# Kernel optimization log

Hardware: AMD Instinct MI355X
Metric: run time of the kernel (lower is better)

Reference implementation:

```python
import jax, jax.numpy as jnp
import numpy as np

K = 16       # hidden size k
STATE = 8    # state_size

def _pre(x, W1, b1, W2, b2):
    # PreProcess: two Linear+ReLU layers
    return jax.nn.relu(jax.nn.relu(x @ W1 + b1) @ W2 + b2)

def _dblock(x, W1, b1, W2, b2, Wmu, bmu, Wls, bls):
    # DBlock (TD-VAE style): gated hidden then mu / logsigma heads
    t = jnp.tanh(x @ W1 + b1) * jax.nn.sigmoid(x @ W2 + b2)
    return t @ Wmu + bmu, t @ Wls + bls

def setup_inputs() -> dict:
    key = jax.random.key(0)
    ks = iter(jax.random.split(key, 40))
    L, B, IN, OBS = 1000, 1024, 8, 4
    def w(shape):
        return (jax.random.normal(next(ks), shape, jnp.float32) / np.sqrt(shape[0])).astype(jnp.float32)
    z = lambda n: jnp.zeros((n,), jnp.float32)
    return {
        "external_input_seq": jax.random.normal(next(ks), (L, B, IN), jnp.float32),
        "observations_seq":   jax.random.normal(next(ks), (L, B, OBS), jnp.float32),
        "eps":                jax.random.normal(next(ks), (L, B, STATE), jnp.float32),
        # process_u / process_x / process_z (PreProcess)
        "pu_W1": w((IN, K)),  "pu_b1": z(K), "pu_W2": w((K, K)), "pu_b2": z(K),
        "px_W1": w((OBS, K)), "px_b1": z(K), "px_W2": w((K, K)), "px_b2": z(K),
        "pz_W1": w((STATE, K)), "pz_b1": z(K), "pz_W2": w((K, K)), "pz_b2": z(K),
        # posterior_gauss: DBlock(3k, 3k, state_size)
        "post_W1": w((3*K, 3*K)), "post_b1": z(3*K),
        "post_W2": w((3*K, 3*K)), "post_b2": z(3*K),
        "post_Wmu": w((3*K, STATE)), "post_bmu": z(STATE),
        "post_Wls": w((3*K, STATE)), "post_bls": z(STATE),
        # rnn: tanh RNN cell, input 3k -> hidden k, 1 layer
        "rnn_Wih": w((3*K, K)), "rnn_bih": z(K),
        "rnn_Whh": w((K, K)),   "rnn_bhh": z(K),
    }

def reference(external_input_seq, observations_seq, eps,
              pu_W1, pu_b1, pu_W2, pu_b2,
              px_W1, px_b1, px_W2, px_b2,
              pz_W1, pz_b1, pz_W2, pz_b2,
              post_W1, post_b1, post_W2, post_b2,
              post_Wmu, post_bmu, post_Wls, post_bls,
              rnn_Wih, rnn_bih, rnn_Whh, rnn_bhh):
    # forward_posterior with memory_state=None
    L, B, _ = external_input_seq.shape
    u_e = _pre(external_input_seq, pu_W1, pu_b1, pu_W2, pu_b2)  # [L,B,K] (precomputed, as in torch)
    x_e = _pre(observations_seq, px_W1, px_b1, px_W2, px_b2)    # [L,B,K]
    h0 = jnp.zeros((B, K), external_input_seq.dtype)

    def step(h, inputs):
        xe_t, ue_t, eps_t = inputs  # [B,K],[B,K],[B,STATE]
        mu, ls = _dblock(jnp.concatenate([xe_t, ue_t, h], -1),
                         post_W1, post_b1, post_W2, post_b2,
                         post_Wmu, post_bmu, post_Wls, post_bls)
        # reparameterized sample from N(mu, diag(exp(ls))) -> std = exp(0.5*ls)
        z_t = mu + jnp.exp(0.5 * ls) * eps_t
        z_e = _pre(z_t, pz_W1, pz_b1, pz_W2, pz_b2)
        rnn_in = jnp.concatenate([xe_t, ue_t, z_e], -1)  # [B,3K]
        h_new = jnp.tanh(rnn_in @ rnn_Wih + rnn_bih + h @ rnn_Whh + rnn_bhh)
        return h_new, (mu, ls)

    h_final, (state_mu, state_logsigma) = jax.lax.scan(step, h0, (x_e, u_e, eps))
    # returns (state_mu, state_logsigma, memory_state hn); rnn_hidden == hn[None] for 1 layer
    return state_mu, state_logsigma, h_final
```

## Files before the change

kernel.cpp:

```cpp
#include <hip/hip_runtime.h>

#define L_STEPS 1000
#define BATCH   1024
#define REC     128

__device__ __forceinline__ float frcp(float x)  { return __builtin_amdgcn_rcpf(x); }
__device__ __forceinline__ float fsig(float x)  { return frcp(1.0f + __expf(-x)); }
__device__ __forceinline__ float ftanh(float x) { return 1.0f - 2.0f * frcp(__expf(2.0f * x) + 1.0f); }

__device__ __forceinline__ float qxor1(float x) {
    return __int_as_float(__builtin_amdgcn_update_dpp(0, __float_as_int(x), 0xB1, 0xF, 0xF, true));
}
__device__ __forceinline__ float qxor2(float x) {
    return __int_as_float(__builtin_amdgcn_update_dpp(0, __float_as_int(x), 0x4E, 0xF, 0xF, true));
}

#define FMA4(vv, W, base, A) do { \
    A = fmaf((vv).x, W[(base)+0], A); \
    A = fmaf((vv).y, W[(base)+1], A); \
    A = fmaf((vv).z, W[(base)+2], A); \
    A = fmaf((vv).w, W[(base)+3], A); } while (0)

__global__ __launch_bounds__(128) void vrnn_pre(
    const float* __restrict__ ext, const float* __restrict__ obs,
    const float* __restrict__ puW1, const float* __restrict__ pub1,
    const float* __restrict__ puW2, const float* __restrict__ pub2,
    const float* __restrict__ pxW1, const float* __restrict__ pxb1,
    const float* __restrict__ pxW2, const float* __restrict__ pxb2,
    const float* __restrict__ poW1, const float* __restrict__ pob1,
    const float* __restrict__ poW2, const float* __restrict__ pob2,
    const float* __restrict__ Wih, const float* __restrict__ bih,
    const float* __restrict__ bhh,
    float* __restrict__ ws)
{
    const int j  = threadIdx.x;
    const int rc = blockIdx.x * 128;
    const int t  = blockIdx.y;

    __shared__ float wsm[768];
    __shared__ float xu[128][36];

    for (int i = j; i < 64;  i += 128) wsm[0   + i] = pxW1[i];
    for (int i = j; i < 256; i += 128) wsm[64  + i] = pxW2[i];
    for (int i = j; i < 128; i += 128) wsm[320 + i] = puW1[i];
    for (int i = j; i < 256; i += 128) wsm[448 + i] = puW2[i];
    if (j < 16) {
        wsm[704 + j] = pxb1[j]; wsm[720 + j] = pxb2[j];
        wsm[736 + j] = pub1[j]; wsm[752 + j] = pub2[j];
    }
    __syncthreads();

    {
        const size_t row = (size_t)t * BATCH + rc + j;
        const float* o = obs + row * 4;
        const float* e = ext + row * 8;
        float ob[4], ex[8];
        #pragma unroll
        for (int k = 0; k < 4; ++k) ob[k] = o[k];
        #pragma unroll
        for (int k = 0; k < 8; ++k) ex[k] = e[k];

        float t1[16];
        #pragma unroll
        for (int c = 0; c < 16; ++c) {
            float a = wsm[704 + c];
            #pragma unroll
            for (int k = 0; k < 4; ++k) a = fmaf(ob[k], wsm[0 + k * 16 + c], a);
            t1[c] = fmaxf(a, 0.0f);
        }
        #pragma unroll
        for (int c = 0; c < 16; ++c) {
            float a = wsm[720 + c];
            #pragma unroll
            for (int k = 0; k < 16; ++k) a = fmaf(t1[k], wsm[64 + k * 16 + c], a);
            xu[j][c] = fmaxf(a, 0.0f);
        }
        #pragma unroll
        for (int c = 0; c < 16; ++c) {
            float a = wsm[736 + c];
            #pragma unroll
            for (int k = 0; k < 8; ++k) a = fmaf(ex[k], wsm[320 + k * 16 + c], a);
            t1[c] = fmaxf(a, 0.0f);
        }
        #pragma unroll
        for (int c = 0; c < 16; ++c) {
            float a = wsm[752 + c];
            #pragma unroll
            for (int k = 0; k < 16; ++k) a = fmaf(t1[k], wsm[448 + k * 16 + c], a);
            xu[j][16 + c] = fmaxf(a, 0.0f);
        }
    }

    float wc[32]; float bias = 0.0f;
    if (j < 96) {
        const int c = j >> 1;
        const float* W = (j & 1) ? poW2 : poW1;
        bias = (j & 1) ? pob2[c] : pob1[c];
        #pragma unroll
        for (int k = 0; k < 32; ++k) wc[k] = W[k * 48 + c];
    } else if (j < 112) {
        const int c = j - 96;
        bias = bih[c] + bhh[c];
        #pragma unroll
        for (int k = 0; k < 32; ++k) wc[k] = Wih[k * 16 + c];
    } else {
        #pragma unroll
        for (int k = 0; k < 32; ++k) wc[k] = 0.0f;
    }
    __syncthreads();

    float* rb = ws + ((size_t)t * BATCH + rc) * REC + j;
    for (int r = 0; r < 128; ++r) {
        const float4* x4 = (const float4*)&xu[r][0];
        float a = bias;
        #pragma unroll
        for (int q = 0; q < 8; ++q) { float4 v = x4[q]; FMA4(v, wc, 4 * q, a); }
        rb[(size_t)r * REC] = a;
    }
}

__global__ __launch_bounds__(64, 1) void vrnn_scan2(
    const float* __restrict__ ws, const float* __restrict__ eps,
    const float* __restrict__ poW1, const float* __restrict__ poW2,
    const float* __restrict__ Wmu, const float* __restrict__ bmu,
    const float* __restrict__ Wls, const float* __restrict__ bls,
    const float* __restrict__ pzW1, const float* __restrict__ pzb1,
    const float* __restrict__ pzW2, const float* __restrict__ pzb2,
    const float* __restrict__ Wih, const float* __restrict__ Whh,
    float* __restrict__ out)
{
    const int l   = threadIdx.x;
    const int r   = blockIdx.x;
    const int idx = l >> 2;
    const int p   = l & 3;

    const int cl = (l < 48) ? l : 47;
    float wAh[16], wBh[16];
    #pragma unroll
    for (int k = 0; k < 16; ++k) {
        wAh[k] = poW1[(32 + k) * 48 + cl];
        wBh[k] = poW2[(32 + k) * 48 + cl];
    }
    const int hm = idx & 7;
    const float* WH = (idx < 8) ? Wmu : Wls;
    float whead[12];
    #pragma unroll
    for (int i = 0; i < 12; ++i) whead[i] = WH[(12 * p + i) * 8 + hm];
    const float bhead = (idx < 8) ? bmu[hm] : bls[hm];

    float wr[8];
    #pragma unroll
    for (int i = 0; i < 8; ++i)
        wr[i] = (p < 2) ? Wih[(32 + 8 * (p & 1) + i) * 16 + idx]
                        : Whh[(8 * (p & 1) + i) * 16 + idx];

    const float wz1a = pzW1[(2 * p) * 16 + idx];
    const float wz1b = pzW1[(2 * p + 1) * 16 + idx];
    const float bz1  = pzb1[idx];
    float wz2[4];
    #pragma unroll
    for (int i = 0; i < 4; ++i) wz2[i] = pzW2[(4 * p + i) * 16 + idx];
    const float bz2 = pzb2[idx];

    const float* recp = ws + (size_t)r * REC + ((l < 48) ? 2 * l : 48 + l);
    const size_t rstride = (size_t)BATCH * REC;
    const float* epsp = eps + (size_t)r * 8 + (l & 7);

    float2 f2 = make_float2(0.0f, 0.0f); float d1 = 0.0f;
    if (l < 48) f2 = *(const float2*)recp; else d1 = *recp;
    float ev = *epsp;
    recp += rstride; epsp += (size_t)8 * BATCH;

    float* pout = out + ((idx < 8) ? ((size_t)r * 8 + idx)
                                   : ((size_t)L_STEPS * BATCH * 8 + (size_t)r * 8 + (idx - 8)));

    float h[16];
    #pragma unroll
    for (int k = 0; k < 16; ++k) h[k] = 0.0f;
    float hn = 0.0f;

    for (int t = 0; t < L_STEPS; ++t) {
        const float s1p = f2.x, s2p = f2.y;
        const float ihpv = d1, epsv = ev;

        float2 nf2 = make_float2(0.0f, 0.0f); float nd1 = 0.0f;
        if (l < 48) nf2 = *(const float2*)recp; else nd1 = *recp;
        float nev = *epsp;
        recp += (t < L_STEPS - 2) ? rstride : 0;
        epsp += (t < L_STEPS - 2) ? (size_t)8 * BATCH : 0;

        const float ihg = __shfl(ihpv, 48 + idx);
        const float eg  = __shfl(epsv, idx & 7);

        #pragma unroll
        for (int k = 0; k < 16; ++k) h[k] = __shfl(hn, 4 * k);
        float sA = s1p, sB = s2p;
        #pragma unroll
        for (int k = 0; k < 16; ++k) {
            sA = fmaf(h[k], wAh[k], sA);
            sB = fmaf(h[k], wBh[k], sB);
        }
        const float tt = ftanh(sA) * fsig(sB);

        float acc = 0.0f;
        #pragma unroll
        for (int i = 0; i < 12; ++i) acc = fmaf(__shfl(tt, 12 * p + i), whead[i], acc);
        acc += qxor1(acc); acc += qxor2(acc);
        acc += bhead;
        if (p == 0) *pout = acc;
        pout += (size_t)8 * BATCH;

        const float other = __shfl(acc, l ^ 32);
        const float zv = fmaf(__expf(0.5f * other), eg, acc);

        float a1 = fmaf(__shfl(zv, 8 * p), wz1a, __shfl(zv, 8 * p + 4) * wz1b);
        a1 += qxor1(a1); a1 += qxor2(a1);
        a1 = fmaxf(a1 + bz1, 0.0f);

        float ze = 0.0f;
        #pragma unroll
        for (int i = 0; i < 4; ++i) ze = fmaf(__shfl(a1, 16 * p + 4 * i), wz2[i], ze);
        ze += qxor1(ze); ze += qxor2(ze);
        ze = fmaxf(ze + bz2, 0.0f);

        float pre = 0.0f;
        #pragma unroll
        for (int i = 0; i < 8; ++i) {
            const float g = __shfl(ze, 4 * (8 * (p & 1) + i));
            const float v = (p < 2) ? g : h[8 * (p & 1) + i];
            pre = fmaf(v, wr[i], pre);
        }
        pre += qxor1(pre); pre += qxor2(pre);
        hn = ftanh(pre + ihg);

        f2 = nf2; d1 = nd1; ev = nev;
    }

    if (p == 0) out[(size_t)L_STEPS * BATCH * 8 * 2 + (size_t)r * 16 + idx] = hn;
}

__global__ __launch_bounds__(64, 1) void vrnn_scan(
    const float* __restrict__ ext, const float* __restrict__ obs, const float* __restrict__ eps,
    const float* __restrict__ puW1, const float* __restrict__ pub1,
    const float* __restrict__ puW2, const float* __restrict__ pub2,
    const float* __restrict__ pxW1, const float* __restrict__ pxb1,
    const float* __restrict__ pxW2, const float* __restrict__ pxb2,
    const float* __restrict__ pzW1, const float* __restrict__ pzb1,
    const float* __restrict__ pzW2, const float* __restrict__ pzb2,
    const float* __restrict__ poW1, const float* __restrict__ pob1,
    const float* __restrict__ poW2, const float* __restrict__ pob2,
    const float* __restrict__ Wmu, const float* __restrict__ bmu,
    const float* __restrict__ Wls, const float* __restrict__ bls,
    const float* __restrict__ Wih, const float* __restrict__ bih,
    const float* __restrict__ Whh, const float* __restrict__ bhh,
    float* __restrict__ out)
{
    const int l   = threadIdx.x;
    const int r   = blockIdx.x;
    const int idx = l >> 2;
    const int p   = l & 3;

    __shared__ __align__(16) float rawbuf[16];
    __shared__ __align__(16) float epsbuf[8];
    __shared__ __align__(16) float h1buf[32];
    __shared__ __align__(16) float in64[64];
    __shared__ __align__(16) float s2buf[48];
    __shared__ __align__(16) float t48[48];
    __shared__ __align__(16) float zbuf[8];
    __shared__ __align__(16) float ze1buf[16];
    __shared__ float bheadb[16];
    __shared__ float brnnb[16];

    if (l < 16) {
        rawbuf[l]    = 0.0f;
        in64[48 + l] = 0.0f;
        bheadb[l]    = (l < 8) ? bmu[l] : bls[l - 8];
        brnnb[l]     = bih[l] + bhh[l];
    }

    float wA[48]; float biasA;
    {
        const float* baseA;
        if (l < 48) { baseA = poW1 + l;        biasA = pob1[l]; }
        else        { baseA = poW2 + (l - 48); biasA = pob2[l - 48]; }
        #pragma unroll
        for (int k = 0; k < 48; ++k) wA[k] = baseA[k * 48];
    }
    float wB[48]; float biasB;
    {
        const int c = 16 + (l & 31);
        const float* baseB = poW2 + c;
        biasB = pob2[c];
        #pragma unroll
        for (int k = 0; k < 48; ++k) wB[k] = baseB[k * 48];
    }
    float whead[12];
    {
        const float* baseH = (idx < 8) ? (Wmu + idx) : (Wls + (idx - 8));
        #pragma unroll
        for (int i = 0; i < 12; ++i) whead[i] = baseH[(12 * p + i) * 8];
    }
    float wrnn[16];
    {
        #pragma unroll
        for (int i = 0; i < 16; ++i) {
            const int c = 16 * p + i;
            const float a = Wih[min(c, 47) * 16 + idx];
            const float b = Whh[max(c - 48, 0) * 16 + idx];
            wrnn[i] = (c < 48) ? a : b;
        }
    }
    const int j16 = l & 15;
    float wpre1[8], wpre2[16], bpre1, bpre2;
    {
        const bool isx = (l < 16);
        #pragma unroll
        for (int k = 0; k < 8; ++k) {
            const float xv = pxW1[min(k, 3) * 16 + j16];
            const float uv = puW1[k * 16 + j16];
            float v = isx ? xv : uv;
            if (isx && k >= 4) v = 0.0f;
            wpre1[k] = v;
        }
        #pragma unroll
        for (int k = 0; k < 16; ++k) {
            const float xv = pxW2[k * 16 + j16];
            const float uv = puW2[k * 16 + j16];
            wpre2[k] = isx ? xv : uv;
        }
        bpre1 = isx ? pxb1[j16] : pub1[j16];
        bpre2 = isx ? pxb2[j16] : pub2[j16];
    }
    float wpz1[8], wpz2[16], bpz1, bpz2;
    {
        #pragma unroll
        for (int k = 0; k < 8; ++k)  wpz1[k] = pzW1[k * 16 + j16];
        #pragma unroll
        for (int k = 0; k < 16; ++k) wpz2[k] = pzW2[k * 16 + j16];
        bpz1 = pzb1[j16];
        bpz2 = pzb2[j16];
    }

    const float* pin; long pstride;
    if (l < 4)                  { pin = obs + (size_t)r * 4 + l;        pstride = 4 * BATCH; }
    else if (l >= 8 && l < 16)  { pin = ext + (size_t)r * 8 + (l - 8);  pstride = 8 * BATCH; }
    else if (l >= 16 && l < 24) { pin = eps + (size_t)r * 8 + (l - 16); pstride = 8 * BATCH; }
    else                        { pin = obs;                            pstride = 0; }

    float vin = *pin;
    pin += pstride;

    float* pout = out + ((idx < 8) ? ((size_t)r * 8 + idx)
                                   : ((size_t)L_STEPS * BATCH * 8 + (size_t)r * 8 + (idx - 8)));

    __syncthreads();

    float hn = 0.0f;

    for (int t = 0; t < L_STEPS; ++t) {
        if (l < 4 || (l >= 8 && l < 16)) rawbuf[l] = vin;
        if (l >= 16 && l < 24)           epsbuf[l - 16] = vin;
        vin = *pin;
        pin += (t < L_STEPS - 2) ? pstride : 0;

        {
            const float4* rb = (const float4*)(rawbuf + ((l & 16) ? 8 : 0));
            float4 v0 = rb[0], v1 = rb[1];
            float a1 = bpre1;
            FMA4(v0, wpre1, 0, a1);
            FMA4(v1, wpre1, 4, a1);
            a1 = fmaxf(a1, 0.0f);
            if (l < 32) h1buf[l] = a1;
            const float4* hb = (const float4*)(h1buf + ((l & 16) ? 16 : 0));
            float a2 = bpre2;
            #pragma unroll
            for (int q = 0; q < 4; ++q) { float4 v = hb[q]; FMA4(v, wpre2, 4 * q, a2); }
            a2 = fmaxf(a2, 0.0f);
            if (l < 32) in64[l] = a2;
        }

        float sA = biasA, sB = biasB;
        {
            const float4* c4 = (const float4*)in64;
            #pragma unroll
            for (int q = 0; q < 8; ++q) {
                float4 v = c4[q];
                FMA4(v, wA, 4 * q, sA);
                FMA4(v, wB, 4 * q, sB);
            }
            const float4* h4 = (const float4*)(in64 + 48);
            #pragma unroll
            for (int q = 0; q < 4; ++q) {
                float4 v = h4[q];
                FMA4(v, wA, 32 + 4 * q, sA);
                FMA4(v, wB, 32 + 4 * q, sB);
            }
        }
        if (l >= 48) s2buf[l - 48] = sA;
        if (l < 32)  s2buf[16 + l] = sB;
        if (l < 48)  t48[l] = ftanh(sA) * fsig(s2buf[l]);

        float acc = 0.0f;
        {
            const float4* tb = (const float4*)(t48 + 12 * p);
            float4 a0 = tb[0], a1v = tb[1], a2v = tb[2];
            FMA4(a0,  whead, 0, acc);
            FMA4(a1v, whead, 4, acc);
            FMA4(a2v, whead, 8, acc);
        }
        acc += __shfl_xor(acc, 1);
        acc += __shfl_xor(acc, 2);
        acc += bheadb[idx];
        if (p == 0) *pout = acc;
        pout += (size_t)8 * BATCH;

        {
            float lsv = __shfl(acc, l | 32);
            if (l < 32) {
                float z = fmaf(__expf(0.5f * lsv), epsbuf[idx], acc);
                if (p == 0) zbuf[idx] = z;
            }
        }

        {
            const float4* zb = (const float4*)zbuf;
            float4 z0 = zb[0], z1 = zb[1];
            float a1 = bpz1;
            FMA4(z0, wpz1, 0, a1);
            FMA4(z1, wpz1, 4, a1);
            a1 = fmaxf(a1, 0.0f);
            if (l < 16) ze1buf[l] = a1;
            const float4* zeb = (const float4*)ze1buf;
            float a2 = bpz2;
            #pragma unroll
            for (int q = 0; q < 4; ++q) { float4 v = zeb[q]; FMA4(v, wpz2, 4 * q, a2); }
            a2 = fmaxf(a2, 0.0f);
            if (l < 16) in64[32 + l] = a2;
        }

        {
            const float4* ib = (const float4*)(in64 + 16 * p);
            float a = 0.0f;
            #pragma unroll
            for (int q = 0; q < 4; ++q) { float4 v = ib[q]; FMA4(v, wrnn, 4 * q, a); }
            a += __shfl_xor(a, 1);
            a += __shfl_xor(a, 2);
            a += brnnb[idx];
            hn = ftanh(a);
            if (p == 0) in64[48 + idx] = hn;
        }
    }

    if (p == 0) out[(size_t)L_STEPS * BATCH * 8 * 2 + (size_t)r * 16 + idx] = hn;
}

extern "C" void kernel_launch(void* const* d_in, const int* in_sizes, int n_in,
                              void* d_out, int out_size, void* d_ws, size_t ws_size,
                              hipStream_t stream) {
    const float* ext  = (const float*)d_in[0];
    const float* obs  = (const float*)d_in[1];
    const float* eps  = (const float*)d_in[2];
    const float* puW1 = (const float*)d_in[3];  const float* pub1 = (const float*)d_in[4];
    const float* puW2 = (const float*)d_in[5];  const float* pub2 = (const float*)d_in[6];
    const float* pxW1 = (const float*)d_in[7];  const float* pxb1 = (const float*)d_in[8];
    const float* pxW2 = (const float*)d_in[9];  const float* pxb2 = (const float*)d_in[10];
    const float* pzW1 = (const float*)d_in[11]; const float* pzb1 = (const float*)d_in[12];
    const float* pzW2 = (const float*)d_in[13]; const float* pzb2 = (const float*)d_in[14];
    const float* poW1 = (const float*)d_in[15]; const float* pob1 = (const float*)d_in[16];
    const float* poW2 = (const float*)d_in[17]; const float* pob2 = (const float*)d_in[18];
    const float* Wmu  = (const float*)d_in[19]; const float* bmu  = (const float*)d_in[20];
    const float* Wls  = (const float*)d_in[21]; const float* bls  = (const float*)d_in[22];
    const float* Wih  = (const float*)d_in[23]; const float* bih  = (const float*)d_in[24];
    const float* Whh  = (const float*)d_in[25]; const float* bhh  = (const float*)d_in[26];
    float* out = (float*)d_out;

    const size_t need = (size_t)L_STEPS * BATCH * REC * sizeof(float);
    if (ws_size >= need) {
        float* ws = (float*)d_ws;
        vrnn_pre<<<dim3(BATCH / 128, L_STEPS), dim3(128), 0, stream>>>(
            ext, obs, puW1, pub1, puW2, pub2, pxW1, pxb1, pxW2, pxb2,
            poW1, pob1, poW2, pob2, Wih, bih, bhh, ws);
        vrnn_scan2<<<dim3(BATCH), dim3(64), 0, stream>>>(
            ws, eps, poW1, poW2, Wmu, bmu, Wls, bls,
            pzW1, pzb1, pzW2, pzb2, Wih, Whh, out);
    } else {
        vrnn_scan<<<dim3(BATCH), dim3(64), 0, stream>>>(
            ext, obs, eps,
            puW1, pub1, puW2, pub2,
            pxW1, pxb1, pxW2, pxb2,
            pzW1, pzb1, pzW2, pzb2,
            poW1, pob1, poW2, pob2,
            Wmu, bmu, Wls, bls,
            Wih, bih, Whh, bhh,
            out);
    }
}
```

Baseline: 1.348 ms.

## Chunk precompute/scan over time to fit workspace and shrink record stride

Reduces the per-row precomputed record from 128 to 112 floats, dropping the padded tail columns that were never used, so the write and read traffic is smaller. Splits the time axis into chunks sized to the available workspace and alternates the pre kernel and the scan kernel per chunk. The hidden state is carried between chunks through the workspace. This lets the two-kernel path run even when the workspace cannot hold the full sequence, at the cost of extra launches and state save/restore.

```diff
diff --git a/kernel.cpp b/kernel.cpp
--- a/kernel.cpp
+++ b/kernel.cpp
@@ -2,7 +2,7 @@
 
 #define L_STEPS 1000
 #define BATCH   1024
-#define REC     128
+#define RECF    112
 
 __device__ __forceinline__ float frcp(float x)  { return __builtin_amdgcn_rcpf(x); }
 __device__ __forceinline__ float fsig(float x)  { return frcp(1.0f + __expf(-x)); }
@@ -31,11 +31,11 @@
     const float* __restrict__ poW2, const float* __restrict__ pob2,
     const float* __restrict__ Wih, const float* __restrict__ bih,
     const float* __restrict__ bhh,
-    float* __restrict__ ws)
+    float* __restrict__ rec, int t0)
 {
     const int j  = threadIdx.x;
     const int rc = blockIdx.x * 128;
-    const int t  = blockIdx.y;
+    const int tl = blockIdx.y;
 
     __shared__ float wsm[768];
     __shared__ float xu[128][36];
@@ -51,7 +51,7 @@
     __syncthreads();
 
     {
-        const size_t row = (size_t)t * BATCH + rc + j;
+        const size_t row = (size_t)(t0 + tl) * BATCH + rc + j;
         const float* o = obs + row * 4;
         const float* e = ext + row * 8;
         float ob[4], ex[8];
@@ -103,31 +103,30 @@
         bias = bih[c] + bhh[c];
         #pragma unroll
         for (int k = 0; k < 32; ++k) wc[k] = Wih[k * 16 + c];
-    } else {
-        #pragma unroll
-        for (int k = 0; k < 32; ++k) wc[k] = 0.0f;
     }
     __syncthreads();
 
-    float* rb = ws + ((size_t)t * BATCH + rc) * REC + j;
-    for (int r = 0; r < 128; ++r) {
-        const float4* x4 = (const float4*)&xu[r][0];
-        float a = bias;
-        #pragma unroll
-        for (int q = 0; q < 8; ++q) { float4 v = x4[q]; FMA4(v, wc, 4 * q, a); }
-        rb[(size_t)r * REC] = a;
+    if (j < 112) {
+        float* rb = rec + ((size_t)tl * BATCH + rc) * RECF + j;
+        for (int r = 0; r < 128; ++r) {
+            const float4* x4 = (const float4*)&xu[r][0];
+            float a = bias;
+            #pragma unroll
+            for (int q = 0; q < 8; ++q) { float4 v = x4[q]; FMA4(v, wc, 4 * q, a); }
+            rb[(size_t)r * RECF] = a;
+        }
     }
 }
 
 __global__ __launch_bounds__(64, 1) void vrnn_scan2(
-    const float* __restrict__ ws, const float* __restrict__ eps,
+    const float* __restrict__ rec, float* wsh, const float* __restrict__ eps,
     const float* __restrict__ poW1, const float* __restrict__ poW2,
     const float* __restrict__ Wmu, const float* __restrict__ bmu,
     const float* __restrict__ Wls, const float* __restrict__ bls,
     const float* __restrict__ pzW1, const float* __restrict__ pzb1,
     const float* __restrict__ pzW2, const float* __restrict__ pzb2,
     const float* __restrict__ Wih, const float* __restrict__ Whh,
-    float* __restrict__ out)
+    float* __restrict__ out, int t0, int T)
 {
     const int l   = threadIdx.x;
     const int r   = blockIdx.x;
@@ -162,32 +161,33 @@
     for (int i = 0; i < 4; ++i) wz2[i] = pzW2[(4 * p + i) * 16 + idx];
     const float bz2 = pzb2[idx];
 
-    const float* recp = ws + (size_t)r * REC + ((l < 48) ? 2 * l : 48 + l);
-    const size_t rstride = (size_t)BATCH * REC;
-    const float* epsp = eps + (size_t)r * 8 + (l & 7);
+    const float* recp = rec + (size_t)r * RECF + ((l < 48) ? 2 * l : 48 + l);
+    const size_t rstride = (size_t)BATCH * RECF;
+    const float* epsp = eps + ((size_t)t0 * BATCH + r) * 8 + (l & 7);
 
     float2 f2 = make_float2(0.0f, 0.0f); float d1 = 0.0f;
     if (l < 48) f2 = *(const float2*)recp; else d1 = *recp;
     float ev = *epsp;
     recp += rstride; epsp += (size_t)8 * BATCH;
 
-    float* pout = out + ((idx < 8) ? ((size_t)r * 8 + idx)
+    float* pout = out + (size_t)t0 * BATCH * 8
+                      + ((idx < 8) ? ((size_t)r * 8 + idx)
                                    : ((size_t)L_STEPS * BATCH * 8 + (size_t)r * 8 + (idx - 8)));
 
+    float hn = (t0 == 0) ? 0.0f : wsh[r * 16 + idx];
     float h[16];
     #pragma unroll
     for (int k = 0; k < 16; ++k) h[k] = 0.0f;
-    float hn = 0.0f;
-
-    for (int t = 0; t < L_STEPS; ++t) {
+
+    for (int t = 0; t < T; ++t) {
         const float s1p = f2.x, s2p = f2.y;
         const float ihpv = d1, epsv = ev;
 
         float2 nf2 = make_float2(0.0f, 0.0f); float nd1 = 0.0f;
         if (l < 48) nf2 = *(const float2*)recp; else nd1 = *recp;
         float nev = *epsp;
-        recp += (t < L_STEPS - 2) ? rstride : 0;
-        epsp += (t < L_STEPS - 2) ? (size_t)8 * BATCH : 0;
+        recp += (t < T - 2) ? rstride : 0;
+        epsp += ((t0 + t) < L_STEPS - 2) ? (size_t)8 * BATCH : 0;
 
         const float ihg = __shfl(ihpv, 48 + idx);
         const float eg  = __shfl(epsv, idx & 7);
@@ -236,7 +236,11 @@
         f2 = nf2; d1 = nd1; ev = nev;
     }
 
-    if (p == 0) out[(size_t)L_STEPS * BATCH * 8 * 2 + (size_t)r * 16 + idx] = hn;
+    if (t0 + T >= L_STEPS) {
+        if (p == 0) out[(size_t)L_STEPS * BATCH * 8 * 2 + (size_t)r * 16 + idx] = hn;
+    } else {
+        if (p == 0) wsh[r * 16 + idx] = hn;
+    }
 }
 
 __global__ __launch_bounds__(64, 1) void vrnn_scan(
@@ -474,15 +478,25 @@
     const float* Whh  = (const float*)d_in[25]; const float* bhh  = (const float*)d_in[26];
     float* out = (float*)d_out;
 
-    const size_t need = (size_t)L_STEPS * BATCH * REC * sizeof(float);
-    if (ws_size >= need) {
-        float* ws = (float*)d_ws;
-        vrnn_pre<<<dim3(BATCH / 128, L_STEPS), dim3(128), 0, stream>>>(
-            ext, obs, puW1, pub1, puW2, pub2, pxW1, pxb1, pxW2, pxb2,
-            poW1, pob1, poW2, pob2, Wih, bih, bhh, ws);
-        vrnn_scan2<<<dim3(BATCH), dim3(64), 0, stream>>>(
-            ws, eps, poW1, poW2, Wmu, bmu, Wls, bls,
-            pzW1, pzb1, pzW2, pzb2, Wih, Whh, out);
+    const size_t hfloats = (size_t)BATCH * 16;
+    const size_t perstep = (size_t)BATCH * RECF * sizeof(float);
+    long tc = 0;
+    if (ws_size > hfloats * sizeof(float))
+        tc = (long)((ws_size - hfloats * sizeof(float)) / perstep);
+    if (tc > L_STEPS) tc = L_STEPS;
+
+    if (tc >= 1) {
+        float* wsh = (float*)d_ws;
+        float* rec = wsh + hfloats;
+        for (int t0 = 0; t0 < L_STEPS; t0 += (int)tc) {
+            const int T = (L_STEPS - t0 < (int)tc) ? (L_STEPS - t0) : (int)tc;
+            vrnn_pre<<<dim3(BATCH / 128, T), dim3(128), 0, stream>>>(
+                ext, obs, puW1, pub1, puW2, pub2, pxW1, pxb1, pxW2, pxb2,
+                poW1, pob1, poW2, pob2, Wih, bih, bhh, rec, t0);
+            vrnn_scan2<<<dim3(BATCH), dim3(64), 0, stream>>>(
+                rec, wsh, eps, poW1, poW2, Wmu, bmu, Wls, bls,
+                pzW1, pzb1, pzW2, pzb2, Wih, Whh, out, t0, T);
+        }
     } else {
         vrnn_scan<<<dim3(BATCH), dim3(64), 0, stream>>>(
             ext, obs, eps,
```

New measurement: 2.235 ms. 1.66x slower.
